# Kernel tuning notes

Measured on AMD Instinct MI355X. Metric: run time of the kernel, lower is better.

## Reference

```python
import jax, jax.numpy as jnp
import numpy as np

TEMPERATURE = 0.07
IGNORE_LABEL = -1
EPS = 1e-8


def setup_inputs() -> dict:
    key = jax.random.key(0)
    k1, k2, k3 = jax.random.split(key, 3)
    N = 100000
    E = 6400000
    edge_index = jax.random.randint(k1, (2, E), 0, N, dtype=jnp.int64)
    edge_logits = jax.random.normal(k2, (E,), dtype=jnp.float32)
    label = jax.random.randint(k3, (N,), 0, 20, dtype=jnp.int64)
    return {"edge_index": edge_index, "edge_logits": edge_logits, "label": label}


def reference(edge_index, edge_logits, label):
    N = label.shape[0]
    idx_i = edge_index[0]
    idx_j = edge_index[1]
    label_i = label[idx_i]
    label_j = label[idx_j]
    valid = (label_i != IGNORE_LABEL) & (label_j != IGNORE_LABEL)
    is_pos = (label_i == label_j) & valid
    is_neg = (label_i != label_j) & valid

    # node is a boundary node if it has at least one valid negative edge
    neg_count = jax.ops.segment_sum(is_neg.astype(jnp.float32), idx_i, num_segments=N)
    is_boundary = (neg_count > 0) & (label != IGNORE_LABEL)

    # edges whose source node is a boundary node (torch filters invalid edges first)
    edge_is_boundary = is_boundary[idx_i] & valid
    exp_logits = jnp.exp(edge_logits / TEMPERATURE)
    w = jnp.where(edge_is_boundary, exp_logits, 0.0)

    denominator = jax.ops.segment_sum(w, idx_i, num_segments=N)
    numerator = jax.ops.segment_sum(jnp.where(is_pos, w, 0.0), idx_i, num_segments=N)

    valid_boundary = is_boundary & (denominator > 0)
    per_node = jnp.where(
        valid_boundary,
        jnp.log(denominator + EPS) - jnp.log(numerator + EPS),
        0.0,
    )
    count = jnp.maximum(jnp.sum(valid_boundary.astype(jnp.float32)), 1.0)
    return jnp.sum(per_node) / count
```

## Files before the change

kernel.cpp:

```cpp
#include <hip/hip_runtime.h>
#include <hip/hip_fp16.h>

#define INV_T  (1.0f / 0.07f)
#define EPS    1e-8f

#define RSH     11
#define RNODES  (1 << RSH)
#define GSPLIT  32
#define SBLK    256
#define EPT     8
#define EPB     (SBLK * EPT)
#define MAXB    256
#define LINV    31u

__global__ void cbl_pack_lab5(const int* __restrict__ label,
                              unsigned char* __restrict__ lab5, int N) {
    int i = blockIdx.x * blockDim.x + threadIdx.x;
    if (i < N) {
        int v = label[i];
        lab5[i] = (v >= 0 && v < 31) ? (unsigned char)v : (unsigned char)LINV;
    }
}

__global__ __launch_bounds__(SBLK) void cbl_scatter(
    const int* __restrict__ idx_i,
    const int* __restrict__ idx_j,
    const float* __restrict__ logits,
    const unsigned char* __restrict__ lab5,
    unsigned* __restrict__ table,
    unsigned* __restrict__ payload,
    int E, int B) {
    __shared__ unsigned s_cnt[4][MAXB];
    __shared__ unsigned s_wb[4][MAXB];
    __shared__ unsigned s_tot[MAXB];
    __shared__ unsigned s_pref[MAXB];
    __shared__ __align__(16) unsigned s_stage[EPB];

    const int wave = threadIdx.x >> 6;
    const int lane = threadIdx.x & 63;

    for (int t = threadIdx.x; t < B; t += SBLK) {
        s_cnt[0][t] = 0; s_cnt[1][t] = 0; s_cnt[2][t] = 0; s_cnt[3][t] = 0;
    }
    __syncthreads();

    const int blockStart = blockIdx.x * EPB;
    int      barr[EPT];
    unsigned marr[EPT];

#pragma unroll
    for (int q = 0; q < EPT / 4; ++q) {
        int base = blockStart + (q * SBLK + threadIdx.x) * 4;
        if (base < E) {
            int4   ii = *reinterpret_cast<const int4*>(idx_i + base);
            int4   jj = *reinterpret_cast<const int4*>(idx_j + base);
            float4 lg = *reinterpret_cast<const float4*>(logits + base);
            int iv[4] = {ii.x, ii.y, ii.z, ii.w};
            int jv[4] = {jj.x, jj.y, jj.z, jj.w};
            float lv[4] = {lg.x, lg.y, lg.z, lg.w};
#pragma unroll
            for (int r = 0; r < 4; ++r) {
                unsigned lj = lab5[jv[r]];
                unsigned hb = (lj != LINV)
                    ? (unsigned)__half_as_ushort(__float2half(lv[r] * INV_T))
                    : 0xFC00u;
                marr[q * 4 + r] = (hb << 16) | (lj << 11)
                                | ((unsigned)iv[r] & (RNODES - 1));
                int b = (iv[r] >> RSH) & (MAXB - 1);
                barr[q * 4 + r] = b;
                atomicAdd(&s_cnt[wave][b], 1u);
            }
        } else {
#pragma unroll
            for (int r = 0; r < 4; ++r) barr[q * 4 + r] = -1;
        }
    }
    __syncthreads();

    for (int t = threadIdx.x; t < B; t += SBLK)
        s_tot[t] = s_cnt[0][t] + s_cnt[1][t] + s_cnt[2][t] + s_cnt[3][t];
    __syncthreads();

    if (B <= 64) {
        if (threadIdx.x < 64) {
            unsigned v = (lane < B) ? s_tot[lane] : 0u;
            unsigned incl = v;
            for (int off = 1; off < 64; off <<= 1) {
                unsigned n = __shfl_up(incl, off, 64);
                if (lane >= off) incl += n;
            }
            if (lane < B) s_pref[lane] = incl - v;
        }
    } else {
        if (threadIdx.x == 0) {
            unsigned r = 0;
            for (int b = 0; b < B; ++b) { s_pref[b] = r; r += s_tot[b]; }
        }
    }
    __syncthreads();

    for (int t = threadIdx.x; t < B; t += SBLK) {
        unsigned pref = s_pref[t];
        table[(size_t)blockIdx.x * B + t] = (pref << 16) | s_tot[t];
        unsigned gb = pref;
        s_wb[0][t] = gb;  gb += s_cnt[0][t];
        s_wb[1][t] = gb;  gb += s_cnt[1][t];
        s_wb[2][t] = gb;  gb += s_cnt[2][t];
        s_wb[3][t] = gb;
        s_cnt[0][t] = 0; s_cnt[1][t] = 0; s_cnt[2][t] = 0; s_cnt[3][t] = 0;
    }
    __syncthreads();

#pragma unroll
    for (int k = 0; k < EPT; ++k) {
        int b = barr[k];
        if (b < 0) continue;
        unsigned slot = s_wb[wave][b] + atomicAdd(&s_cnt[wave][b], 1u);
        s_stage[slot] = marr[k];
    }
    __syncthreads();

    int lim = E - blockStart; if (lim > EPB) lim = EPB;
    int lim4 = lim >> 2;
    const uint4* src4 = reinterpret_cast<const uint4*>(s_stage);
    uint4* dst4 = reinterpret_cast<uint4*>(payload + blockStart);
    for (int t = threadIdx.x; t < lim4; t += SBLK) dst4[t] = src4[t];
}

__global__ __launch_bounds__(256) void cbl_accum(
    const unsigned* __restrict__ payload,
    const unsigned* __restrict__ table,
    const unsigned char* __restrict__ lab5,
    float* __restrict__ partials,
    int N, int B, int nBlk) {
    int b = blockIdx.x / GSPLIT;
    int g = blockIdx.x % GSPLIT;

    __shared__ float         acc[RNODES * 2];
    __shared__ unsigned char slab[RNODES];

    for (int t = threadIdx.x; t < RNODES * 2; t += 256) acc[t] = 0.0f;
    int nodeBase = b << RSH;
    for (int t = threadIdx.x; t < RNODES; t += 256) {
        int n = nodeBase + t;
        slab[t] = (n < N) ? lab5[n] : (unsigned char)LINV;
    }
    __syncthreads();

    int wave = threadIdx.x >> 6, lane = threadIdx.x & 63;
    for (int c = g * 4 + wave; c < nBlk; c += GSPLIT * 4) {
        unsigned tbl  = table[(size_t)c * B + b];
        unsigned cnt  = tbl & 0xFFFFu;
        unsigned start = (unsigned)c * EPB + (tbl >> 16);
        for (unsigned k = lane; k < cnt; k += 64) {
            unsigned p = payload[start + k];
            unsigned local = p & (RNODES - 1);
            unsigned lj    = (p >> 11) & 31u;
            unsigned li    = slab[local];
            float x = __half2float(__ushort_as_half((unsigned short)(p >> 16)));
            float w = (li == LINV) ? 0.0f : __expf(x);
            atomicAdd(&acc[(local << 1) | (li == lj ? 1u : 0u)], w);
        }
    }
    __syncthreads();

    float* dst = partials + (size_t)blockIdx.x * (RNODES * 2);
    for (int t = threadIdx.x; t < RNODES * 2; t += 256) dst[t] = acc[t];
}

__global__ __launch_bounds__(256) void cbl_loss(
    const float* __restrict__ partials,
    float* __restrict__ acc2, int N) {
    float lsum = 0.0f, lcnt = 0.0f;
    int stride = gridDim.x * blockDim.x;
    for (int n = blockIdx.x * blockDim.x + threadIdx.x; n < N; n += stride) {
        int b = n >> RSH;
        int local = n & (RNODES - 1);
        float neg = 0.0f, pos = 0.0f;
#pragma unroll 4
        for (int g = 0; g < GSPLIT; ++g) {
            const float* p = partials
                + (size_t)(b * GSPLIT + g) * (RNODES * 2) + local * 2;
            float2 v = *reinterpret_cast<const float2*>(p);
            neg += v.x;
            pos += v.y;
        }
        if (neg > 0.0f) {
            lsum += logf(neg + pos + EPS) - logf(pos + EPS);
            lcnt += 1.0f;
        }
    }
    for (int off = 32; off > 0; off >>= 1) {
        lsum += __shfl_down(lsum, off, 64);
        lcnt += __shfl_down(lcnt, off, 64);
    }
    __shared__ float s_sum[4];
    __shared__ float s_cnt2[4];
    int wid = threadIdx.x >> 6, lane = threadIdx.x & 63;
    if (lane == 0) { s_sum[wid] = lsum; s_cnt2[wid] = lcnt; }
    __syncthreads();
    if (threadIdx.x == 0) {
        float bs = 0.0f, bc = 0.0f;
        for (int w = 0; w < 4; ++w) { bs += s_sum[w]; bc += s_cnt2[w]; }
        atomicAdd(&acc2[0], bs);
        atomicAdd(&acc2[1], bc);
    }
}

__global__ void cbl_finalize(const float* __restrict__ acc2,
                             float* __restrict__ out) {
    out[0] = acc2[0] / fmaxf(acc2[1], 1.0f);
}

__global__ __launch_bounds__(256) void cbl_edge_fb(
    const int* __restrict__ idx_i, const int* __restrict__ idx_j,
    const float* __restrict__ logits, const unsigned char* __restrict__ lab5,
    float* __restrict__ buf, int E) {
    int stride = gridDim.x * blockDim.x;
    for (int e = blockIdx.x * blockDim.x + threadIdx.x; e < E; e += stride) {
        unsigned li = lab5[idx_i[e]];
        unsigned lj = lab5[idx_j[e]];
        if (li == LINV || lj == LINV) continue;
        float w = __expf(logits[e] * INV_T);
        int slot = (idx_i[e] << 1) | (li == lj ? 1 : 0);
        atomicAdd(&buf[slot], w);
    }
}

__global__ __launch_bounds__(256) void cbl_loss_fb(
    const float* __restrict__ buf, float* __restrict__ acc2, int N) {
    float lsum = 0.0f, lcnt = 0.0f;
    int stride = gridDim.x * blockDim.x;
    for (int n = blockIdx.x * blockDim.x + threadIdx.x; n < N; n += stride) {
        float neg = buf[2 * n], pos = buf[2 * n + 1];
        if (neg > 0.0f) {
            lsum += logf(neg + pos + EPS) - logf(pos + EPS);
            lcnt += 1.0f;
        }
    }
    for (int off = 32; off > 0; off >>= 1) {
        lsum += __shfl_down(lsum, off, 64);
        lcnt += __shfl_down(lcnt, off, 64);
    }
    __shared__ float s_sum[4];
    __shared__ float s_cnt2[4];
    int wid = threadIdx.x >> 6, lane = threadIdx.x & 63;
    if (lane == 0) { s_sum[wid] = lsum; s_cnt2[wid] = lcnt; }
    __syncthreads();
    if (threadIdx.x == 0) {
        float bs = 0.0f, bc = 0.0f;
        for (int w = 0; w < 4; ++w) { bs += s_sum[w]; bc += s_cnt2[w]; }
        atomicAdd(&acc2[0], bs);
        atomicAdd(&acc2[1], bc);
    }
}

extern "C" void kernel_launch(void* const* d_in, const int* in_sizes, int n_in,
                              void* d_out, int out_size, void* d_ws, size_t ws_size,
                              hipStream_t stream) {
    const int*   edge_index = (const int*)d_in[0];
    const float* logits     = (const float*)d_in[1];
    const int*   label      = (const int*)d_in[2];

    const int E = in_sizes[1];
    const int N = in_sizes[2];
    const int* idx_i = edge_index;
    const int* idx_j = edge_index + E;

    const int B    = (N + RNODES - 1) >> RSH;
    const int nBlk = (E + EPB - 1) / EPB;
    const int block = 256;

    char* p = (char*)d_ws;
    float*    acc2   = (float*)p;               p += 16;
    unsigned char* lab5 = (unsigned char*)p;    p += ((size_t)N + 15) & ~(size_t)15;
    unsigned* table  = (unsigned*)p;            p += (((size_t)nBlk * B * 4) + 15) & ~(size_t)15;
    unsigned* payload = (unsigned*)p;           p += (((size_t)E * 4) + 15) & ~(size_t)15;
    float*    partials = (float*)p;             p += (size_t)B * GSPLIT * RNODES * 2 * 4;
    size_t need = (size_t)(p - (char*)d_ws);

    const bool fast = (ws_size >= need) && ((E & 3) == 0) && (E >= 4) &&
                      (B >= 1) && (B <= MAXB) &&
                      (((uintptr_t)payload & 15) == 0);

    if (fast) {
        hipMemsetAsync(acc2, 0, 8, stream);
        cbl_pack_lab5<<<(N + block - 1) / block, block, 0, stream>>>(label, lab5, N);

        cbl_scatter<<<nBlk, SBLK, 0, stream>>>(idx_i, idx_j, logits, lab5,
                                               table, payload, E, B);

        cbl_accum<<<B * GSPLIT, block, 0, stream>>>(payload, table, lab5,
                                                    partials, N, B, nBlk);

        int g5 = (N + block - 1) / block; if (g5 > 1024) g5 = 1024;
        cbl_loss<<<g5, block, 0, stream>>>(partials, acc2, N);
        cbl_finalize<<<1, 1, 0, stream>>>(acc2, (float*)d_out);
    } else {
        float* buf = (float*)d_ws;
        float* facc = buf + (size_t)2 * N;
        unsigned char* flab = (unsigned char*)(facc + 2);
        hipMemsetAsync(d_ws, 0, (size_t)N * 8 + 8, stream);
        cbl_pack_lab5<<<(N + block - 1) / block, block, 0, stream>>>(label, flab, N);
        int ge = (E + block - 1) / block; if (ge > 8192) ge = 8192;
        cbl_edge_fb<<<ge, block, 0, stream>>>(idx_i, idx_j, logits, flab, buf, E);
        int g5 = (N + block - 1) / block; if (g5 > 1024) g5 = 1024;
        cbl_loss_fb<<<g5, block, 0, stream>>>(buf, facc, N);
        cbl_finalize<<<1, 1, 0, stream>>>(facc, (float*)d_out);
    }
}
```

Baseline: 105.0 us.

## Transpose bucket table and batch four source chunks per wave in accumulation

Stores the per-block bucket table transposed (bucket-major, padded to a multiple of four blocks) so the accumulate kernel can read four consecutive chunk descriptors with one 16-byte load. Each wave now walks the concatenation of four chunks in a single lane-strided loop, improving lane utilisation since each chunk holds only a few dozen edges. Adds a per-element select chain for address computation and launches a few padded scatter blocks that write empty entries.

```diff
diff --git a/kernel.cpp b/kernel.cpp
--- a/kernel.cpp
+++ b/kernel.cpp
@@ -27,9 +27,9 @@
     const int* __restrict__ idx_j,
     const float* __restrict__ logits,
     const unsigned char* __restrict__ lab5,
-    unsigned* __restrict__ table,
+    unsigned* __restrict__ table_t,
     unsigned* __restrict__ payload,
-    int E, int B) {
+    int E, int B, int nBlkPad) {
     __shared__ unsigned s_cnt[4][MAXB];
     __shared__ unsigned s_wb[4][MAXB];
     __shared__ unsigned s_tot[MAXB];
@@ -101,7 +101,7 @@
 
     for (int t = threadIdx.x; t < B; t += SBLK) {
         unsigned pref = s_pref[t];
-        table[(size_t)blockIdx.x * B + t] = (pref << 16) | s_tot[t];
+        table_t[(size_t)t * nBlkPad + blockIdx.x] = (pref << 16) | s_tot[t];
         unsigned gb = pref;
         s_wb[0][t] = gb;  gb += s_cnt[0][t];
         s_wb[1][t] = gb;  gb += s_cnt[1][t];
@@ -129,10 +129,10 @@
 
 __global__ __launch_bounds__(256) void cbl_accum(
     const unsigned* __restrict__ payload,
-    const unsigned* __restrict__ table,
+    const unsigned* __restrict__ table_t,
     const unsigned char* __restrict__ lab5,
     float* __restrict__ partials,
-    int N, int B, int nBlk) {
+    int N, int B, int nBlkPad) {
     int b = blockIdx.x / GSPLIT;
     int g = blockIdx.x % GSPLIT;
 
@@ -148,12 +148,26 @@
     __syncthreads();
 
     int wave = threadIdx.x >> 6, lane = threadIdx.x & 63;
-    for (int c = g * 4 + wave; c < nBlk; c += GSPLIT * 4) {
-        unsigned tbl  = table[(size_t)c * B + b];
-        unsigned cnt  = tbl & 0xFFFFu;
-        unsigned start = (unsigned)c * EPB + (tbl >> 16);
-        for (unsigned k = lane; k < cnt; k += 64) {
-            unsigned p = payload[start + k];
+    int ngroups = nBlkPad >> 2;
+    const unsigned* trow = table_t + (size_t)b * nBlkPad;
+
+    for (int gg = g * 4 + wave; gg < ngroups; gg += GSPLIT * 4) {
+        unsigned c0 = (unsigned)gg * 4u;
+        uint4 t4 = *reinterpret_cast<const uint4*>(trow + c0);
+        unsigned cnt0 = t4.x & 0xFFFFu, cnt1 = t4.y & 0xFFFFu;
+        unsigned cnt2 = t4.z & 0xFFFFu, cnt3 = t4.w & 0xFFFFu;
+        unsigned s0 = c0 * EPB + (t4.x >> 16);
+        unsigned s1 = (c0 + 1) * EPB + (t4.y >> 16);
+        unsigned s2 = (c0 + 2) * EPB + (t4.z >> 16);
+        unsigned s3 = (c0 + 3) * EPB + (t4.w >> 16);
+        unsigned p1 = cnt0, p2 = p1 + cnt1, p3 = p2 + cnt2;
+        unsigned total = p3 + cnt3;
+        for (unsigned k = lane; k < total; k += 64) {
+            unsigned addr = (k < p1) ? (s0 + k)
+                          : (k < p2) ? (s1 + (k - p1))
+                          : (k < p3) ? (s2 + (k - p2))
+                          :            (s3 + (k - p3));
+            unsigned p = payload[addr];
             unsigned local = p & (RNODES - 1);
             unsigned lj    = (p >> 11) & 31u;
             unsigned li    = slab[local];
@@ -267,31 +281,33 @@
     const int* idx_i = edge_index;
     const int* idx_j = edge_index + E;
 
-    const int B    = (N + RNODES - 1) >> RSH;
-    const int nBlk = (E + EPB - 1) / EPB;
-    const int block = 256;
+    const int B       = (N + RNODES - 1) >> RSH;
+    const int nBlk    = (E + EPB - 1) / EPB;
+    const int nBlkPad = (nBlk + 3) & ~3;
+    const int block   = 256;
 
     char* p = (char*)d_ws;
     float*    acc2   = (float*)p;               p += 16;
     unsigned char* lab5 = (unsigned char*)p;    p += ((size_t)N + 15) & ~(size_t)15;
-    unsigned* table  = (unsigned*)p;            p += (((size_t)nBlk * B * 4) + 15) & ~(size_t)15;
+    unsigned* table_t = (unsigned*)p;           p += (((size_t)B * nBlkPad * 4) + 15) & ~(size_t)15;
     unsigned* payload = (unsigned*)p;           p += (((size_t)E * 4) + 15) & ~(size_t)15;
     float*    partials = (float*)p;             p += (size_t)B * GSPLIT * RNODES * 2 * 4;
     size_t need = (size_t)(p - (char*)d_ws);
 
     const bool fast = (ws_size >= need) && ((E & 3) == 0) && (E >= 4) &&
                       (B >= 1) && (B <= MAXB) &&
-                      (((uintptr_t)payload & 15) == 0);
+                      (((uintptr_t)payload & 15) == 0) &&
+                      (((uintptr_t)table_t & 15) == 0);
 
     if (fast) {
         hipMemsetAsync(acc2, 0, 8, stream);
         cbl_pack_lab5<<<(N + block - 1) / block, block, 0, stream>>>(label, lab5, N);
 
-        cbl_scatter<<<nBlk, SBLK, 0, stream>>>(idx_i, idx_j, logits, lab5,
-                                               table, payload, E, B);
-
-        cbl_accum<<<B * GSPLIT, block, 0, stream>>>(payload, table, lab5,
-                                                    partials, N, B, nBlk);
+        cbl_scatter<<<nBlkPad, SBLK, 0, stream>>>(idx_i, idx_j, logits, lab5,
+                                                  table_t, payload, E, B, nBlkPad);
+
+        cbl_accum<<<B * GSPLIT, block, 0, stream>>>(payload, table_t, lab5,
+                                                    partials, N, B, nBlkPad);
 
         int g5 = (N + block - 1) / block; if (g5 > 1024) g5 = 1024;
         cbl_loss<<<g5, block, 0, stream>>>(partials, acc2, N);
```

New measurement: 107.2 us. 2.1% more time.
